# Kernel tuning notes

Measured on AMD Instinct MI355X. Metric: run time of the kernel, lower is better.

Reference implementation:

```python
import jax, jax.numpy as jnp
import numpy as np

K, S, B, D = 6, 257, 64, 1024   # blocks, seq, batch, d_model
H, DR = 16, 256                  # heads, pruned dim (d_model/reduction)
HD = DR // H                     # head_dim = 16
T = 0.1
EPS = 1e-5


def _ln(x, w, b):
    mu = jnp.mean(x, axis=-1, keepdims=True)
    var = jnp.var(x, axis=-1, keepdims=True)
    return (x - mu) * jax.lax.rsqrt(var + EPS) * w + b


def _quick_gelu(x):
    return x * jax.nn.sigmoid(1.702 * x)


def _block(x, ipw, ipb, opw, opb, l1w, l1b, l2w, l2b, fw, fb, cw, cb):
    # x: (S, B, D)
    h = _ln(x, l1w, l1b)
    qkv = jnp.einsum('sbe,fe->sbf', h, ipw) + ipb          # (S, B, 3*DR)
    q, k, v = jnp.split(qkv, 3, axis=-1)                    # each (S, B, DR)
    # (S, B*H, HD) -> (B*H, S, HD); row-major reshape matches torch .view
    q = q.reshape(S, B * H, HD).swapaxes(0, 1) / jnp.sqrt(jnp.asarray(HD, x.dtype))
    k = k.reshape(S, B * H, HD).swapaxes(0, 1)
    v = v.reshape(S, B * H, HD).swapaxes(0, 1)
    attn = jax.nn.softmax(jnp.einsum('bte,bse->bts', q, k), axis=-1)  # (B*H, S, S)
    o = jnp.einsum('bts,bse->bte', attn, v)                 # (B*H, S, HD)
    o = o.swapaxes(0, 1).reshape(S, B, DR)
    o = jnp.einsum('sbe,fe->sbf', o, opw) + opb             # (S, B, D)
    x = x + o
    h2 = _ln(x, l2w, l2b)
    m = _quick_gelu(jnp.einsum('sbe,fe->sbf', h2, fw) + fb)
    m = jnp.einsum('sbe,fe->sbf', m, cw) + cb
    return x + m


def setup_inputs() -> dict:
    key = jax.random.key(0)
    ks = jax.random.split(key, 10)
    p = 0.02
    return {
        'hook_inputs': jax.random.normal(ks[0], (K, S, B, D), jnp.float32),
        'alpha': jax.random.normal(ks[1], (K,), jnp.float32),
        'in_proj_w': jax.random.normal(ks[2], (K, 3 * DR, D), jnp.float32) * p,
        'in_proj_b': jnp.zeros((K, 3 * DR), jnp.float32),
        'out_proj_w': jax.random.normal(ks[3], (K, D, DR), jnp.float32) * p,
        'out_proj_b': jnp.zeros((K, D), jnp.float32),
        'ln1_w': jnp.ones((K, D), jnp.float32),
        'ln1_b': jnp.zeros((K, D), jnp.float32),
        'ln2_w': jnp.ones((K, D), jnp.float32),
        'ln2_b': jnp.zeros((K, D), jnp.float32),
        'fc_w': jax.random.normal(ks[4], (K, D, D), jnp.float32) * p,
        'fc_b': jnp.zeros((K, D), jnp.float32),
        'cproj_w': jax.random.normal(ks[5], (K, D, D), jnp.float32) * p,
        'cproj_b': jnp.zeros((K, D), jnp.float32),
        'ln_post_w': jnp.ones((D,), jnp.float32),
        'ln_post_b': jnp.zeros((D,), jnp.float32),
        'proj': jax.random.normal(ks[6], (D, 768), jnp.float32) * p,
    }


def reference(hook_inputs, alpha, in_proj_w, in_proj_b, out_proj_w, out_proj_b,
              ln1_w, ln1_b, ln2_w, ln2_b, fc_w, fc_b, cproj_w, cproj_b,
              ln_post_w, ln_post_b, proj):
    Wm = jax.nn.sigmoid(alpha / T)
    x = None
    for i in range(K):  # small fixed number of structurally distinct blocks
        res = hook_inputs[i]
        if i == 0:
            x = res
        else:
            x = Wm[i] * res + (1.0 - Wm[i]) * x
        x = _block(x, in_proj_w[i], in_proj_b[i], out_proj_w[i], out_proj_b[i],
                   ln1_w[i], ln1_b[i], ln2_w[i], ln2_b[i],
                   fc_w[i], fc_b[i], cproj_w[i], cproj_b[i])
    x = x.transpose(1, 0, 2)                 # (B, S, D)
    x = _ln(x, ln_post_w, ln_post_b)
    x = jnp.einsum('bsd,dp->bsp', x, proj)   # (B, S, 768)
    return x
```

## Files before the change

kernel.cpp:

```cpp
#include <hip/hip_runtime.h>
#include <hip/hip_bf16.h>
#include <cstdint>
#include <cstddef>

#define KBLK 6
#define SL 257
#define BA 64
#define DM 1024
#define NHEAD 16
#define DRED 256
#define HDM 16
#define MR (SL * BA)
#define MP 16512
#define LNEPS 1e-5f

typedef __hip_bfloat16 bf16;
typedef __attribute__((ext_vector_type(8))) short short8;
typedef __attribute__((ext_vector_type(4))) short short4_t;
typedef __attribute__((ext_vector_type(4))) float f32x4;

__device__ __forceinline__ void gld_lds16(const void* g, void* l) {
  __builtin_amdgcn_global_load_lds(
      (const __attribute__((address_space(1))) unsigned int*)g,
      (__attribute__((address_space(3))) unsigned int*)l, 16, 0, 0);
}

__device__ __forceinline__ float bf2f(short s) {
  bf16 t = *reinterpret_cast<bf16*>(&s);
  return __bfloat162float(t);
}
__device__ __forceinline__ short f2bf(float f) {
  bf16 t = __float2bfloat16(f);
  return *reinterpret_cast<short*>(&t);
}

__global__ __launch_bounds__(256) void cast_all_kernel(
    const float* __restrict__ ipw, const float* __restrict__ opw,
    const float* __restrict__ fcw, const float* __restrict__ cpw,
    const float* __restrict__ proj,
    bf16* __restrict__ wq, bf16* __restrict__ wo, bf16* __restrict__ wfc,
    bf16* __restrict__ wcp, bf16* __restrict__ wpj) {
  const int blk = blockIdx.x;
  const int tid = threadIdx.x;
  const float* src;
  bf16* dst;
  int base;
  bool tr = false;
  if (blk < 2304)      { src = ipw; dst = wq;  base = blk * 2048; }
  else if (blk < 3072) { src = opw; dst = wo;  base = (blk - 2304) * 2048; }
  else if (blk < 6144) { src = fcw; dst = wfc; base = (blk - 3072) * 2048; }
  else if (blk < 9216) { src = cpw; dst = wcp; base = (blk - 6144) * 2048; }
  else                 { src = proj; dst = wpj; base = (blk - 9216) * 2048; tr = true; }
  const int idx = base + tid * 8;
  short8 o;
  if (!tr) {
    float4 a = *(const float4*)(src + idx);
    float4 b = *(const float4*)(src + idx + 4);
    o[0] = f2bf(a.x); o[1] = f2bf(a.y); o[2] = f2bf(a.z); o[3] = f2bf(a.w);
    o[4] = f2bf(b.x); o[5] = f2bf(b.y); o[6] = f2bf(b.z); o[7] = f2bf(b.w);
  } else {
    int n = idx >> 10, k = idx & 1023;
#pragma unroll
    for (int e = 0; e < 8; ++e) o[e] = f2bf(src[(size_t)(k + e) * 768 + n]);
  }
  *(short8*)(dst + idx) = o;
}

template <int MODE>
__global__ __launch_bounds__(256) void ln_kernel(
    const float* __restrict__ hook,
    bf16* __restrict__ x, bf16* __restrict__ hout,
    const float* __restrict__ w, const float* __restrict__ bb) {
  const int row = blockIdx.x;
  const int tid = threadIdx.x;
  const size_t base = (size_t)row * DM + tid * 4;
  float vals[4];
  if (MODE == 0) {
    float4 v = *(const float4*)(hook + base);
    vals[0] = v.x; vals[1] = v.y; vals[2] = v.z; vals[3] = v.w;
    short4_t pk;
#pragma unroll
    for (int j = 0; j < 4; ++j) pk[j] = f2bf(vals[j]);
    *(short4_t*)&x[base] = pk;
  } else {
    short4_t xv = *(const short4_t*)&x[base];
#pragma unroll
    for (int j = 0; j < 4; ++j) vals[j] = bf2f(xv[j]);
  }
  float s1 = vals[0] + vals[1] + vals[2] + vals[3];
  float s2 = vals[0] * vals[0] + vals[1] * vals[1] + vals[2] * vals[2] + vals[3] * vals[3];
#pragma unroll
  for (int o = 32; o >= 1; o >>= 1) {
    s1 += __shfl_down(s1, o);
    s2 += __shfl_down(s2, o);
  }
  __shared__ float red[8];
  if ((tid & 63) == 0) {
    red[tid >> 6] = s1;
    red[4 + (tid >> 6)] = s2;
  }
  __syncthreads();
  s1 = red[0] + red[1] + red[2] + red[3];
  s2 = red[4] + red[5] + red[6] + red[7];
  const float mu = s1 * (1.f / DM);
  const float rs = rsqrtf(s2 * (1.f / DM) - mu * mu + LNEPS);
  size_t orow = row;
  if (MODE == 3) {
    int s = row >> 6, b2 = row & 63;
    orow = (size_t)b2 * SL + s;
  }
  const int c = tid * 4;
  short4_t pk;
#pragma unroll
  for (int j = 0; j < 4; ++j)
    pk[j] = f2bf((vals[j] - mu) * rs * w[c + j] + bb[c + j]);
  *(short4_t*)((char*)hout + (orow * DM + c) * 2) = pk;
}

__global__ __launch_bounds__(256) void attn_mfma_kernel(const bf16* __restrict__ qkv,
                                                        bf16* __restrict__ obuf) {
  __shared__ __align__(16) short ql[272][24];
  __shared__ __align__(16) short kl[272][24];
  __shared__ __align__(16) short vt[16][296];
  __shared__ __align__(16) short pl[4][16][40];
  const int bh = blockIdx.x;
  const int b = bh >> 4, h = bh & 15;
  const int tid = threadIdx.x;
  const int wave = tid >> 6, lane = tid & 63;
  const int g = lane >> 4, qi = lane & 15;

  const short8 zero8 = {0, 0, 0, 0, 0, 0, 0, 0};
  const f32x4 fzero = {0.f, 0.f, 0.f, 0.f};

  for (int task = tid; task < 1632; task += 256) {
    int a, rem;
    if (task < 544) { a = 0; rem = task; }
    else if (task < 1088) { a = 1; rem = task - 544; }
    else { a = 2; rem = task - 1088; }
    int row = rem >> 1, half = rem & 1;
    short8 v = zero8;
    if (row < SL)
      v = *(const short8*)((const short*)qkv + (size_t)(row * BA + b) * 768 + a * 256 + h * 16 + half * 8);
    if (a == 0) *(short8*)&ql[row][half * 8] = v;
    else if (a == 1) *(short8*)&kl[row][half * 8] = v;
    else {
#pragma unroll
      for (int j = 0; j < 8; ++j) vt[half * 8 + j][row] = v[j];
    }
  }
  for (int i = tid; i < 16 * 24; i += 256) vt[i / 24][272 + (i % 24)] = 0;
  __syncthreads();

  for (int t = wave; t < 17; t += 4) {
    short8 bq = zero8;
    if (g < 2) bq = *(const short8*)&ql[t * 16 + qi][g * 8];

    f32x4 st[18];
#pragma unroll
    for (int t2 = 0; t2 < 17; ++t2) {
      short8 ak = zero8;
      if (g < 2) ak = *(const short8*)&kl[t2 * 16 + qi][g * 8];
      st[t2] = __builtin_amdgcn_mfma_f32_16x16x32_bf16(ak, bq, fzero, 0, 0, 0);
    }
    float mx = -1e30f;
#pragma unroll
    for (int t2 = 0; t2 < 17; ++t2) {
#pragma unroll
      for (int r = 0; r < 4; ++r) {
        int s = t2 * 16 + g * 4 + r;
        float v = (s <= 256) ? st[t2][r] * 0.25f : -1e30f;
        st[t2][r] = v;
        mx = fmaxf(mx, v);
      }
    }
    mx = fmaxf(mx, __shfl_xor(mx, 16));
    mx = fmaxf(mx, __shfl_xor(mx, 32));
    float ls = 0.f;
#pragma unroll
    for (int t2 = 0; t2 < 17; ++t2) {
#pragma unroll
      for (int r = 0; r < 4; ++r) {
        float p = __expf(st[t2][r] - mx);
        st[t2][r] = p;
        ls += p;
      }
    }
    ls += __shfl_xor(ls, 16);
    ls += __shfl_xor(ls, 32);
    const float inv = 1.f / ls;
#pragma unroll
    for (int t2 = 0; t2 < 17; ++t2)
#pragma unroll
      for (int r = 0; r < 4; ++r) st[t2][r] *= inv;
    st[17] = fzero;

    f32x4 acc = fzero;
#pragma unroll
    for (int tt = 0; tt < 9; ++tt) {
#pragma unroll
      for (int hh = 0; hh < 2; ++hh) {
        int t2 = tt * 2 + hh;
        short4_t pk;
#pragma unroll
        for (int r = 0; r < 4; ++r) pk[r] = f2bf(st[t2][r]);
        *(short4_t*)&pl[wave][qi][hh * 16 + g * 4] = pk;
      }
      short8 pa = *(const short8*)&pl[wave][qi][g * 8];
      short8 bv = *(const short8*)&vt[qi][tt * 32 + g * 8];
      acc = __builtin_amdgcn_mfma_f32_16x16x32_bf16(pa, bv, acc, 0, 0, 0);
    }
#pragma unroll
    for (int r = 0; r < 4; ++r) {
      int qr = t * 16 + g * 4 + r;
      if (qr < SL)
        obuf[(size_t)(qr * BA + b) * DRED + h * 16 + qi] = __float2bfloat16(acc[r]);
    }
  }
}

template <int EPI, int KDIM, int NT>
__global__ __launch_bounds__(256, 4) void gemm_kernel(
    const bf16* __restrict__ A, int lda,
    const bf16* __restrict__ Bw, int ldb,
    const float* __restrict__ bias,
    void* __restrict__ C, int ldc,
    const float* __restrict__ hook, const float* __restrict__ alphap, int kidx) {
  __shared__ char lds[32768];
  const int tid = threadIdx.x;
  const int wave = tid >> 6, lane = tid & 63;
  const int lrow = lane & 15, lk = lane >> 4;
  const int wr = wave >> 1, wc = wave & 1;

  constexpr int nwg = 129 * NT;
  constexpr int q = nwg >> 3, r = nwg & 7;
  const int orig = blockIdx.y * 129 + blockIdx.x;
  const int xcd = orig & 7, idx = orig >> 3;
  const int wgid = (xcd < r ? xcd * (q + 1) : r * (q + 1) + (xcd - r) * q) + idx;
  const int m0 = (wgid / NT) * 128;
  const int n0 = (wgid % NT) * 128;

  f32x4 acc[4][4];
  const f32x4 zero = {0.f, 0.f, 0.f, 0.f};
#pragma unroll
  for (int i = 0; i < 4; ++i)
#pragma unroll
    for (int j = 0; j < 4; ++j) acc[i][j] = zero;

  constexpr int nk = KDIM >> 6;

  for (int kt = 0; kt < nk; ++kt) {
    const int k0 = kt << 6;
#pragma unroll
    for (int j = 0; j < 4; ++j) {
      int c = wave * 256 + j * 64 + lane;
      int row = c >> 3, segp = c & 7;
      int seg = segp ^ (row & 7);
      gld_lds16(A + (size_t)(m0 + row) * lda + k0 + seg * 8, &lds[c * 16]);
      gld_lds16(Bw + (size_t)(n0 + row) * ldb + k0 + seg * 8, &lds[16384 + c * 16]);
    }
    __syncthreads();
#pragma unroll
    for (int kh = 0; kh < 2; ++kh) {
      short8 af[4], bfr[4];
#pragma unroll
      for (int i = 0; i < 4; ++i) {
        int rr = wr * 64 + i * 16 + lrow;
        int seg = kh * 4 + lk;
        af[i] = *(const short8*)(lds + rr * 128 + ((seg ^ (rr & 7)) << 4));
      }
#pragma unroll
      for (int j = 0; j < 4; ++j) {
        int rr = wc * 64 + j * 16 + lrow;
        int seg = kh * 4 + lk;
        bfr[j] = *(const short8*)(lds + 16384 + rr * 128 + ((seg ^ (rr & 7)) << 4));
      }
#pragma unroll
      for (int i = 0; i < 4; ++i)
#pragma unroll
        for (int j = 0; j < 4; ++j)
          acc[i][j] = __builtin_amdgcn_mfma_f32_16x16x32_bf16(bfr[j], af[i], acc[i][j], 0, 0, 0);
    }
    __syncthreads();
  }

  float wmg = 0.f, omg = 0.f;
  if (EPI == 4) {
    wmg = 1.f / (1.f + __expf(-alphap[kidx] * 10.f));
    omg = 1.f - wmg;
  }
  float4 bj[4];
#pragma unroll
  for (int j = 0; j < 4; ++j) {
    const int col = n0 + wc * 64 + j * 16 + lk * 4;
    bj[j] = bias ? *(const float4*)&bias[col] : float4{0.f, 0.f, 0.f, 0.f};
  }
#pragma unroll
  for (int i = 0; i < 4; ++i) {
    const int row = m0 + wr * 64 + i * 16 + lrow;
    if (row >= MR) continue;
#pragma unroll
    for (int j = 0; j < 4; ++j) {
      const int col = n0 + wc * 64 + j * 16 + lk * 4;
      const size_t off = (size_t)row * ldc + col;
      const float bv[4] = {bj[j].x, bj[j].y, bj[j].z, bj[j].w};
      float v[4];
#pragma unroll
      for (int rr = 0; rr < 4; ++rr) v[rr] = acc[i][j][rr] + bv[rr];
      if (EPI == 0) {
        float4 o4 = {v[0], v[1], v[2], v[3]};
        *(float4*)((float*)C + off) = o4;
      } else if (EPI == 2) {
        short4_t pk;
#pragma unroll
        for (int rr = 0; rr < 4; ++rr)
          pk[rr] = f2bf(v[rr] / (1.f + __expf(-1.702f * v[rr])));
        *(short4_t*)((bf16*)C + off) = pk;
      } else if (EPI == 3) {
        short4_t pk;
#pragma unroll
        for (int rr = 0; rr < 4; ++rr) pk[rr] = f2bf(v[rr]);
        *(short4_t*)((bf16*)C + off) = pk;
      } else if (EPI == 1) {
        short4_t xv = *(const short4_t*)((const bf16*)C + off);
        short4_t pk;
#pragma unroll
        for (int rr = 0; rr < 4; ++rr) pk[rr] = f2bf(bf2f(xv[rr]) + v[rr]);
        *(short4_t*)((bf16*)C + off) = pk;
      } else {
        short4_t xv = *(const short4_t*)((const bf16*)C + off);
        float4 h4 = *(const float4*)&hook[off];
        float hk[4] = {h4.x, h4.y, h4.z, h4.w};
        short4_t pk;
#pragma unroll
        for (int rr = 0; rr < 4; ++rr)
          pk[rr] = f2bf(wmg * hk[rr] + omg * (bf2f(xv[rr]) + v[rr]));
        *(short4_t*)((bf16*)C + off) = pk;
      }
    }
  }
}

extern "C" void kernel_launch(void* const* d_in, const int* in_sizes, int n_in,
                              void* d_out, int out_size, void* d_ws, size_t ws_size,
                              hipStream_t stream) {
  const float* hook = (const float*)d_in[0];
  const float* alpha = (const float*)d_in[1];
  const float* ipw = (const float*)d_in[2];
  const float* ipb = (const float*)d_in[3];
  const float* opw = (const float*)d_in[4];
  const float* opb = (const float*)d_in[5];
  const float* l1w = (const float*)d_in[6];
  const float* l1b = (const float*)d_in[7];
  const float* l2w = (const float*)d_in[8];
  const float* l2b = (const float*)d_in[9];
  const float* fcw = (const float*)d_in[10];
  const float* fcb = (const float*)d_in[11];
  const float* cpw = (const float*)d_in[12];
  const float* cpb = (const float*)d_in[13];
  const float* lpw = (const float*)d_in[14];
  const float* lpb = (const float*)d_in[15];
  const float* proj = (const float*)d_in[16];

  char* ws = (char*)d_ws;
  size_t off = 0;
  bf16* x = (bf16*)(ws + off); off += (size_t)MP * DM * 2;
  bf16* hbuf = (bf16*)(ws + off); off += (size_t)MP * DM * 2;
  bf16* qkv = (bf16*)(ws + off);
  bf16* mbuf = (bf16*)qkv;
  off += (size_t)MP * 1024 * 2;
  bf16* obuf = (bf16*)(ws + off); off += (size_t)MP * DRED * 2;
  bf16* wq = (bf16*)(ws + off); off += (size_t)KBLK * 768 * DM * 2;
  bf16* wo = (bf16*)(ws + off); off += (size_t)KBLK * DM * DRED * 2;
  bf16* wfc = (bf16*)(ws + off); off += (size_t)KBLK * DM * DM * 2;
  bf16* wcp = (bf16*)(ws + off); off += (size_t)KBLK * DM * DM * 2;
  bf16* wpj = (bf16*)(ws + off); off += (size_t)768 * DM * 2;

  cast_all_kernel<<<9600, 256, 0, stream>>>(ipw, opw, fcw, cpw, proj,
                                            wq, wo, wfc, wcp, wpj);

  const dim3 gq(129, 6);
  const dim3 gm(129, 8);

  for (int i = 0; i < KBLK; ++i) {
    if (i == 0)
      ln_kernel<0><<<MR, 256, 0, stream>>>(hook, x, hbuf, l1w, l1b);
    else
      ln_kernel<2><<<MR, 256, 0, stream>>>(nullptr, x, hbuf, l1w + i * DM, l1b + i * DM);
    gemm_kernel<3, 1024, 6><<<gq, 256, 0, stream>>>(hbuf, DM, wq + (size_t)i * 768 * DM, DM,
                                                    ipb + i * 768, qkv, 768,
                                                    nullptr, nullptr, 0);
    attn_mfma_kernel<<<BA * NHEAD, 256, 0, stream>>>(qkv, obuf);
    gemm_kernel<1, 256, 8><<<gm, 256, 0, stream>>>(obuf, DRED, wo + (size_t)i * DM * DRED, DRED,
                                                   opb + i * DM, x, DM,
                                                   nullptr, nullptr, 0);
    ln_kernel<2><<<MR, 256, 0, stream>>>(nullptr, x, hbuf, l2w + i * DM, l2b + i * DM);
    gemm_kernel<2, 1024, 8><<<gm, 256, 0, stream>>>(hbuf, DM, wfc + (size_t)i * DM * DM, DM,
                                                    fcb + i * DM, mbuf, DM,
                                                    nullptr, nullptr, 0);
    if (i + 1 < KBLK)
      gemm_kernel<4, 1024, 8><<<gm, 256, 0, stream>>>(mbuf, DM, wcp + (size_t)i * DM * DM, DM,
                                                      cpb + i * DM, x, DM,
                                                      hook + (size_t)(i + 1) * MR * DM, alpha, i + 1);
    else
      gemm_kernel<1, 1024, 8><<<gm, 256, 0, stream>>>(mbuf, DM, wcp + (size_t)i * DM * DM, DM,
                                                      cpb + i * DM, x, DM,
                                                      nullptr, nullptr, 0);
  }
  ln_kernel<3><<<MR, 256, 0, stream>>>(nullptr, x, hbuf, lpw, lpb);
  gemm_kernel<0, 1024, 6><<<gq, 256, 0, stream>>>(hbuf, DM, wpj, DM, nullptr,
                                                  (float*)d_out, 768,
                                                  nullptr, nullptr, 0);
}
```

Measured before the change: 1.702 ms.

## Fold LayerNorm into GEMM weights and epilogues with atomic row statistics

```diff
diff --git a/kernel.cpp b/kernel.cpp
--- a/kernel.cpp
+++ b/kernel.cpp
@@ -38,57 +38,131 @@
     const float* __restrict__ ipw, const float* __restrict__ opw,
     const float* __restrict__ fcw, const float* __restrict__ cpw,
     const float* __restrict__ proj,
+    const float* __restrict__ l1w, const float* __restrict__ l1b,
+    const float* __restrict__ l2w, const float* __restrict__ l2b,
+    const float* __restrict__ lpw, const float* __restrict__ lpb,
+    const float* __restrict__ ipb, const float* __restrict__ fcb,
     bf16* __restrict__ wq, bf16* __restrict__ wo, bf16* __restrict__ wfc,
-    bf16* __restrict__ wcp, bf16* __restrict__ wpj) {
+    bf16* __restrict__ wcp, bf16* __restrict__ wpj,
+    float* __restrict__ sq_q, float* __restrict__ bb_q,
+    float* __restrict__ sq_fc, float* __restrict__ bb_fc,
+    float* __restrict__ sq_pj, float* __restrict__ bb_pj) {
   const int blk = blockIdx.x;
   const int tid = threadIdx.x;
-  const float* src;
-  bf16* dst;
-  int base;
-  bool tr = false;
-  if (blk < 2304)      { src = ipw; dst = wq;  base = blk * 2048; }
-  else if (blk < 3072) { src = opw; dst = wo;  base = (blk - 2304) * 2048; }
-  else if (blk < 6144) { src = fcw; dst = wfc; base = (blk - 3072) * 2048; }
-  else if (blk < 9216) { src = cpw; dst = wcp; base = (blk - 6144) * 2048; }
-  else                 { src = proj; dst = wpj; base = (blk - 9216) * 2048; tr = true; }
-  const int idx = base + tid * 8;
-  short8 o;
-  if (!tr) {
-    float4 a = *(const float4*)(src + idx);
-    float4 b = *(const float4*)(src + idx + 4);
+  float sp = 0.f, bbp = 0.f;
+  float* sqDst = nullptr;
+  float* bbDst = nullptr;
+  const float* bflat = nullptr;
+  int grow = 0;
+
+  if (blk < 2304) {
+    const int base = blk * 2048, idx = base + tid * 8;
+    grow = base >> 10;
+    const int rowt = idx >> 10, col = idx & 1023;
+    const int tb = rowt / 768;
+    const float* lw = l1w + tb * DM;
+    const float* lb = l1b + tb * DM;
+    float4 a = *(const float4*)(ipw + idx);
+    float4 b = *(const float4*)(ipw + idx + 4);
+    float v[8] = {a.x, a.y, a.z, a.w, b.x, b.y, b.z, b.w};
+    short8 o;
+#pragma unroll
+    for (int e = 0; e < 8; ++e) {
+      float f = v[e] * lw[col + e];
+      sp += f;
+      bbp += lb[col + e] * v[e];
+      o[e] = f2bf(f);
+    }
+    *(short8*)(wq + idx) = o;
+    sqDst = sq_q; bbDst = bb_q; bflat = ipb;
+  } else if (blk < 3072) {
+    const int base = (blk - 2304) * 2048, idx = base + tid * 8;
+    float4 a = *(const float4*)(opw + idx);
+    float4 b = *(const float4*)(opw + idx + 4);
+    short8 o;
     o[0] = f2bf(a.x); o[1] = f2bf(a.y); o[2] = f2bf(a.z); o[3] = f2bf(a.w);
     o[4] = f2bf(b.x); o[5] = f2bf(b.y); o[6] = f2bf(b.z); o[7] = f2bf(b.w);
+    *(short8*)(wo + idx) = o;
+  } else if (blk < 6144) {
+    const int base = (blk - 3072) * 2048, idx = base + tid * 8;
+    grow = base >> 10;
+    const int rowt = idx >> 10, col = idx & 1023;
+    const int tb = rowt >> 10;
+    const float* lw = l2w + tb * DM;
+    const float* lb = l2b + tb * DM;
+    float4 a = *(const float4*)(fcw + idx);
+    float4 b = *(const float4*)(fcw + idx + 4);
+    float v[8] = {a.x, a.y, a.z, a.w, b.x, b.y, b.z, b.w};
+    short8 o;
+#pragma unroll
+    for (int e = 0; e < 8; ++e) {
+      float f = v[e] * lw[col + e];
+      sp += f;
+      bbp += lb[col + e] * v[e];
+      o[e] = f2bf(f);
+    }
+    *(short8*)(wfc + idx) = o;
+    sqDst = sq_fc; bbDst = bb_fc; bflat = fcb;
+  } else if (blk < 9216) {
+    const int base = (blk - 6144) * 2048, idx = base + tid * 8;
+    float4 a = *(const float4*)(cpw + idx);
+    float4 b = *(const float4*)(cpw + idx + 4);
+    short8 o;
+    o[0] = f2bf(a.x); o[1] = f2bf(a.y); o[2] = f2bf(a.z); o[3] = f2bf(a.w);
+    o[4] = f2bf(b.x); o[5] = f2bf(b.y); o[6] = f2bf(b.z); o[7] = f2bf(b.w);
+    *(short8*)(wcp + idx) = o;
   } else {
-    int n = idx >> 10, k = idx & 1023;
-#pragma unroll
-    for (int e = 0; e < 8; ++e) o[e] = f2bf(src[(size_t)(k + e) * 768 + n]);
-  }
-  *(short8*)(dst + idx) = o;
-}
-
-template <int MODE>
-__global__ __launch_bounds__(256) void ln_kernel(
-    const float* __restrict__ hook,
-    bf16* __restrict__ x, bf16* __restrict__ hout,
-    const float* __restrict__ w, const float* __restrict__ bb) {
+    const int base = (blk - 9216) * 2048, idx = base + tid * 8;
+    grow = base >> 10;
+    const int n = idx >> 10, k0 = idx & 1023;
+    short8 o;
+#pragma unroll
+    for (int e = 0; e < 8; ++e) {
+      float v = proj[(size_t)(k0 + e) * 768 + n];
+      float f = v * lpw[k0 + e];
+      sp += f;
+      bbp += lpb[k0 + e] * v;
+      o[e] = f2bf(f);
+    }
+    *(short8*)(wpj + idx) = o;
+    sqDst = sq_pj; bbDst = bb_pj; bflat = nullptr;
+  }
+
+  if (sqDst) {
+#pragma unroll
+    for (int o = 32; o >= 1; o >>= 1) {
+      sp += __shfl_down(sp, o);
+      bbp += __shfl_down(bbp, o);
+    }
+    __shared__ float wred[4][2];
+    const int wave = tid >> 6;
+    if ((tid & 63) == 0) {
+      wred[wave][0] = sp;
+      wred[wave][1] = bbp;
+    }
+    __syncthreads();
+    if (tid == 0) {
+      sqDst[grow] = wred[0][0] + wred[1][0];
+      bbDst[grow] = wred[0][1] + wred[1][1] + (bflat ? bflat[grow] : 0.f);
+    } else if (tid == 128) {
+      sqDst[grow + 1] = wred[2][0] + wred[3][0];
+      bbDst[grow + 1] = wred[2][1] + wred[3][1] + (bflat ? bflat[grow + 1] : 0.f);
+    }
+  }
+}
+
+__global__ __launch_bounds__(256) void stat0_kernel(
+    const float* __restrict__ hook, bf16* __restrict__ x,
+    float2* __restrict__ st12) {
   const int row = blockIdx.x;
   const int tid = threadIdx.x;
   const size_t base = (size_t)row * DM + tid * 4;
-  float vals[4];
-  if (MODE == 0) {
-    float4 v = *(const float4*)(hook + base);
-    vals[0] = v.x; vals[1] = v.y; vals[2] = v.z; vals[3] = v.w;
-    short4_t pk;
-#pragma unroll
-    for (int j = 0; j < 4; ++j) pk[j] = f2bf(vals[j]);
-    *(short4_t*)&x[base] = pk;
-  } else {
-    short4_t xv = *(const short4_t*)&x[base];
-#pragma unroll
-    for (int j = 0; j < 4; ++j) vals[j] = bf2f(xv[j]);
-  }
-  float s1 = vals[0] + vals[1] + vals[2] + vals[3];
-  float s2 = vals[0] * vals[0] + vals[1] * vals[1] + vals[2] * vals[2] + vals[3] * vals[3];
+  float4 v = *(const float4*)(hook + base);
+  short4_t pk;
+  pk[0] = f2bf(v.x); pk[1] = f2bf(v.y); pk[2] = f2bf(v.z); pk[3] = f2bf(v.w);
+  *(short4_t*)&x[base] = pk;
+  float s1 = v.x + v.y + v.z + v.w;
+  float s2 = v.x * v.x + v.y * v.y + v.z * v.z + v.w * v.w;
 #pragma unroll
   for (int o = 32; o >= 1; o >>= 1) {
     s1 += __shfl_down(s1, o);
@@ -100,21 +174,11 @@
     red[4 + (tid >> 6)] = s2;
   }
   __syncthreads();
-  s1 = red[0] + red[1] + red[2] + red[3];
-  s2 = red[4] + red[5] + red[6] + red[7];
-  const float mu = s1 * (1.f / DM);
-  const float rs = rsqrtf(s2 * (1.f / DM) - mu * mu + LNEPS);
-  size_t orow = row;
-  if (MODE == 3) {
-    int s = row >> 6, b2 = row & 63;
-    orow = (size_t)b2 * SL + s;
-  }
-  const int c = tid * 4;
-  short4_t pk;
-#pragma unroll
-  for (int j = 0; j < 4; ++j)
-    pk[j] = f2bf((vals[j] - mu) * rs * w[c + j] + bb[c + j]);
-  *(short4_t*)((char*)hout + (orow * DM + c) * 2) = pk;
+  if (tid == 0) {
+    float t1 = red[0] + red[1] + red[2] + red[3];
+    float t2 = red[4] + red[5] + red[6] + red[7];
+    st12[row] = make_float2(t1, t2);
+  }
 }
 
 __global__ __launch_bounds__(256) void attn_mfma_kernel(const bf16* __restrict__ qkv,
@@ -224,7 +288,10 @@
     const bf16* __restrict__ Bw, int ldb,
     const float* __restrict__ bias,
     void* __restrict__ C, int ldc,
-    const float* __restrict__ hook, const float* __restrict__ alphap, int kidx) {
+    const float* __restrict__ hook, const float* __restrict__ alphap, int kidx,
+    const float2* __restrict__ statsIn,
+    const float* __restrict__ sarr, const float* __restrict__ barr,
+    float2* __restrict__ statsOut) {
   __shared__ char lds[32768];
   const int tid = threadIdx.x;
   const int wave = tid >> 6, lane = tid & 63;
@@ -284,57 +351,78 @@
   }
 
   float wmg = 0.f, omg = 0.f;
-  if (EPI == 4) {
+  if (EPI == 9) {
     wmg = 1.f / (1.f + __expf(-alphap[kidx] * 10.f));
     omg = 1.f - wmg;
   }
-  float4 bj[4];
-#pragma unroll
-  for (int j = 0; j < 4; ++j) {
-    const int col = n0 + wc * 64 + j * 16 + lk * 4;
-    bj[j] = bias ? *(const float4*)&bias[col] : float4{0.f, 0.f, 0.f, 0.f};
-  }
+
 #pragma unroll
   for (int i = 0; i < 4; ++i) {
     const int row = m0 + wr * 64 + i * 16 + lrow;
     if (row >= MR) continue;
-#pragma unroll
-    for (int j = 0; j < 4; ++j) {
-      const int col = n0 + wc * 64 + j * 16 + lk * 4;
-      const size_t off = (size_t)row * ldc + col;
-      const float bv[4] = {bj[j].x, bj[j].y, bj[j].z, bj[j].w};
-      float v[4];
-#pragma unroll
-      for (int rr = 0; rr < 4; ++rr) v[rr] = acc[i][j][rr] + bv[rr];
-      if (EPI == 0) {
-        float4 o4 = {v[0], v[1], v[2], v[3]};
-        *(float4*)((float*)C + off) = o4;
-      } else if (EPI == 2) {
+
+    if (EPI == 5 || EPI == 6 || EPI == 7) {
+      const float2 st = statsIn[row];
+      const float mu = st.x * (1.f / DM);
+      const float rs = rsqrtf(st.y * (1.f / DM) - mu * mu + LNEPS);
+      const float mrs = mu * rs;
+#pragma unroll
+      for (int j = 0; j < 4; ++j) {
+        const int col = n0 + wc * 64 + j * 16 + lk * 4;
+        float4 sp4 = *(const float4*)&sarr[col];
+        float4 bb4 = *(const float4*)&barr[col];
+        float v[4];
+        v[0] = rs * acc[i][j][0] - mrs * sp4.x + bb4.x;
+        v[1] = rs * acc[i][j][1] - mrs * sp4.y + bb4.y;
+        v[2] = rs * acc[i][j][2] - mrs * sp4.z + bb4.z;
+        v[3] = rs * acc[i][j][3] - mrs * sp4.w + bb4.w;
+        if (EPI == 5) {
+          short4_t pk;
+#pragma unroll
+          for (int rr = 0; rr < 4; ++rr) pk[rr] = f2bf(v[rr]);
+          *(short4_t*)((bf16*)C + (size_t)row * ldc + col) = pk;
+        } else if (EPI == 6) {
+          short4_t pk;
+#pragma unroll
+          for (int rr = 0; rr < 4; ++rr)
+            pk[rr] = f2bf(v[rr] / (1.f + __expf(-1.702f * v[rr])));
+          *(short4_t*)((bf16*)C + (size_t)row * ldc + col) = pk;
+        } else {
+          const size_t orow = (size_t)(row & 63) * SL + (row >> 6);
+          float4 o4 = {v[0], v[1], v[2], v[3]};
+          *(float4*)((float*)C + orow * ldc + col) = o4;
+        }
+      }
+    } else {
+      float s1 = 0.f, s2 = 0.f;
+#pragma unroll
+      for (int j = 0; j < 4; ++j) {
+        const int col = n0 + wc * 64 + j * 16 + lk * 4;
+        const size_t off = (size_t)row * ldc + col;
+        float4 b4 = *(const float4*)&bias[col];
+        const float bv[4] = {b4.x, b4.y, b4.z, b4.w};
+        short4_t xv = *(const short4_t*)((const bf16*)C + off);
+        float4 h4;
+        if (EPI == 9) h4 = *(const float4*)&hook[off];
+        const float hk[4] = {h4.x, h4.y, h4.z, h4.w};
         short4_t pk;
 #pragma unroll
-        for (int rr = 0; rr < 4; ++rr)
-          pk[rr] = f2bf(v[rr] / (1.f + __expf(-1.702f * v[rr])));
+        for (int rr = 0; rr < 4; ++rr) {
+          float t = bf2f(xv[rr]) + acc[i][j][rr] + bv[rr];
+          if (EPI == 9) t = wmg * hk[rr] + omg * t;
+          s1 += t;
+          s2 += t * t;
+          pk[rr] = f2bf(t);
+        }
         *(short4_t*)((bf16*)C + off) = pk;
-      } else if (EPI == 3) {
-        short4_t pk;
-#pragma unroll
-        for (int rr = 0; rr < 4; ++rr) pk[rr] = f2bf(v[rr]);
-        *(short4_t*)((bf16*)C + off) = pk;
-      } else if (EPI == 1) {
-        short4_t xv = *(const short4_t*)((const bf16*)C + off);
-        short4_t pk;
-#pragma unroll
-        for (int rr = 0; rr < 4; ++rr) pk[rr] = f2bf(bf2f(xv[rr]) + v[rr]);
-        *(short4_t*)((bf16*)C + off) = pk;
-      } else {
-        short4_t xv = *(const short4_t*)((const bf16*)C + off);
-        float4 h4 = *(const float4*)&hook[off];
-        float hk[4] = {h4.x, h4.y, h4.z, h4.w};
-        short4_t pk;
-#pragma unroll
-        for (int rr = 0; rr < 4; ++rr)
-          pk[rr] = f2bf(wmg * hk[rr] + omg * (bf2f(xv[rr]) + v[rr]));
-        *(short4_t*)((bf16*)C + off) = pk;
+      }
+      s1 += __shfl_xor(s1, 16);
+      s1 += __shfl_xor(s1, 32);
+      s2 += __shfl_xor(s2, 16);
+      s2 += __shfl_xor(s2, 32);
+      if (lk == 0) {
+        atomicAdd(&statsOut[row].x, s1);
+        atomicAdd(&statsOut[row].y, s2);
       }
     }
   }
@@ -364,7 +452,6 @@
   char* ws = (char*)d_ws;
   size_t off = 0;
   bf16* x = (bf16*)(ws + off); off += (size_t)MP * DM * 2;
-  bf16* hbuf = (bf16*)(ws + off); off += (size_t)MP * DM * 2;
   bf16* qkv = (bf16*)(ws + off);
   bf16* mbuf = (bf16*)qkv;
   off += (size_t)MP * 1024 * 2;
@@ -374,40 +461,50 @@
   bf16* wfc = (bf16*)(ws + off); off += (size_t)KBLK * DM * DM * 2;
   bf16* wcp = (bf16*)(ws + off); off += (size_t)KBLK * DM * DM * 2;
   bf16* wpj = (bf16*)(ws + off); off += (size_t)768 * DM * 2;
-
-  cast_all_kernel<<<9600, 256, 0, stream>>>(ipw, opw, fcw, cpw, proj,
-                                            wq, wo, wfc, wcp, wpj);
+  float2* stats = (float2*)(ws + off); off += (size_t)13 * MR * sizeof(float2);
+  float* sq_q = (float*)(ws + off); off += (size_t)KBLK * 768 * 4;
+  float* bb_q = (float*)(ws + off); off += (size_t)KBLK * 768 * 4;
+  float* sq_fc = (float*)(ws + off); off += (size_t)KBLK * DM * 4;
+  float* bb_fc = (float*)(ws + off); off += (size_t)KBLK * DM * 4;
+  float* sq_pj = (float*)(ws + off); off += (size_t)768 * 4;
+  float* bb_pj = (float*)(ws + off); off += (size_t)768 * 4;
+
+  hipMemsetAsync(stats, 0, (size_t)13 * MR * sizeof(float2), stream);
+  cast_all_kernel<<<9600, 256, 0, stream>>>(
+      ipw, opw, fcw, cpw, proj, l1w, l1b, l2w, l2b, lpw, lpb, ipb, fcb,
+      wq, wo, wfc, wcp, wpj, sq_q, bb_q, sq_fc, bb_fc, sq_pj, bb_pj);
+  stat0_kernel<<<MR, 256, 0, stream>>>(hook, x, stats + (size_t)12 * MR);
 
   const dim3 gq(129, 6);
   const dim3 gm(129, 8);
 
   for (int i = 0; i < KBLK; ++i) {
-    if (i == 0)
-      ln_kernel<0><<<MR, 256, 0, stream>>>(hook, x, hbuf, l1w, l1b);
+    const float2* stIn = (i == 0) ? stats + (size_t)12 * MR
+                                  : stats + (size_t)(2 * i - 1) * MR;
+    gemm_kernel<5, 1024, 6><<<gq, 256, 0, stream>>>(
+        x, DM, wq + (size_t)i * 768 * DM, DM, nullptr, qkv, 768,
+        nullptr, nullptr, 0, stIn, sq_q + i * 768, bb_q + i * 768, nullptr);
+    attn_mfma_kernel<<<BA * NHEAD, 256, 0, stream>>>(qkv, obuf);
+    gemm_kernel<8, 256, 8><<<gm, 256, 0, stream>>>(
+        obuf, DRED, wo + (size_t)i * DM * DRED, DRED, opb + i * DM, x, DM,
+        nullptr, nullptr, 0, nullptr, nullptr, nullptr,
+        stats + (size_t)(2 * i) * MR);
+    gemm_kernel<6, 1024, 8><<<gm, 256, 0, stream>>>(
+        x, DM, wfc + (size_t)i * DM * DM, DM, nullptr, mbuf, DM,
+        nullptr, nullptr, 0, stats + (size_t)(2 * i) * MR,
+        sq_fc + i * DM, bb_fc + i * DM, nullptr);
+    if (i + 1 < KBLK)
+      gemm_kernel<9, 1024, 8><<<gm, 256, 0, stream>>>(
+          mbuf, DM, wcp + (size_t)i * DM * DM, DM, cpb + i * DM, x, DM,
+          hook + (size_t)(i + 1) * MR * DM, alpha, i + 1,
+          nullptr, nullptr, nullptr, stats + (size_t)(2 * i + 1) * MR);
     else
-      ln_kernel<2><<<MR, 256, 0, stream>>>(nullptr, x, hbuf, l1w + i * DM, l1b + i * DM);
-    gemm_kernel<3, 1024, 6><<<gq, 256, 0, stream>>>(hbuf, DM, wq + (size_t)i * 768 * DM, DM,
-                                                    ipb + i * 768, qkv, 768,
-                                                    nullptr, nullptr, 0);
-    attn_mfma_kernel<<<BA * NHEAD, 256, 0, stream>>>(qkv, obuf);
-    gemm_kernel<1, 256, 8><<<gm, 256, 0, stream>>>(obuf, DRED, wo + (size_t)i * DM * DRED, DRED,
-                                                   opb + i * DM, x, DM,
-                                                   nullptr, nullptr, 0);
-    ln_kernel<2><<<MR, 256, 0, stream>>>(nullptr, x, hbuf, l2w + i * DM, l2b + i * DM);
-    gemm_kernel<2, 1024, 8><<<gm, 256, 0, stream>>>(hbuf, DM, wfc + (size_t)i * DM * DM, DM,
-                                                    fcb + i * DM, mbuf, DM,
-                                                    nullptr, nullptr, 0);
-    if (i + 1 < KBLK)
-      gemm_kernel<4, 1024, 8><<<gm, 256, 0, stream>>>(mbuf, DM, wcp + (size_t)i * DM * DM, DM,
-                                                      cpb + i * DM, x, DM,
-                                                      hook + (size_t)(i + 1) * MR * DM, alpha, i + 1);
-    else
-      gemm_kernel<1, 1024, 8><<<gm, 256, 0, stream>>>(mbuf, DM, wcp + (size_t)i * DM * DM, DM,
-                                                      cpb + i * DM, x, DM,
-                                                      nullptr, nullptr, 0);
-  }
-  ln_kernel<3><<<MR, 256, 0, stream>>>(nullptr, x, hbuf, lpw, lpb);
-  gemm_kernel<0, 1024, 6><<<gq, 256, 0, stream>>>(hbuf, DM, wpj, DM, nullptr,
-                                                  (float*)d_out, 768,
-                                                  nullptr, nullptr, 0);
-}
+      gemm_kernel<8, 1024, 8><<<gm, 256, 0, stream>>>(
+          mbuf, DM, wcp + (size_t)i * DM * DM, DM, cpb + i * DM, x, DM,
+          nullptr, nullptr, 0, nullptr, nullptr, nullptr,
+          stats + (size_t)(2 * i + 1) * MR);
+  }
+  gemm_kernel<7, 1024, 6><<<gq, 256, 0, stream>>>(
+      x, DM, wpj, DM, nullptr, (float*)d_out, 768,
+      nullptr, nullptr, 0, stats + (size_t)11 * MR, sq_pj, bb_pj, nullptr);
+}
```

Result: faster. 1.607 ms (-5.6%).
